# Optimization experiments

Measured on AMD Instinct MI355X. Metric: run time of the kernel, lower is better.

## Reference

```python
import jax, jax.numpy as jnp
import numpy as np

B_SZ, NP, NTOK, D, H, DH, D2 = 8192, 10, 21, 128, 2, 64, 32
EPS = 1e-8
PATCH_POS = np.array([2 * k - 1 for k in range(1, NP + 1)])  # [1,3,...,19]
STAT_POS = np.array([0] + [2 * k for k in range(1, NP + 1)])  # [0,2,...,20]


def setup_inputs() -> dict:
    key = jax.random.key(0)
    ks = jax.random.split(key, 12)
    x = jax.random.normal(ks[0], (B_SZ, NTOK, D), jnp.float32)
    # rotary frequencies: unit-magnitude complex exp(i * pos * theta)
    inv_freq = 1.0 / (10000.0 ** (jnp.arange(D2, dtype=jnp.float32) / D2))
    ang = jnp.arange(NTOK, dtype=jnp.float32)[:, None] * inv_freq[None, :]  # [N, d2]
    fc_real, fc_imag = jnp.cos(ang), jnp.sin(ang)
    s = 1.0 / np.sqrt(D)
    g = 1.0 + 0.02 * jax.random.normal(ks[1], (D,), jnp.float32)
    Wqkv = s * jax.random.normal(ks[2], (D, 3 * D), jnp.float32)
    bqkv = jnp.zeros((3 * D,), jnp.float32)
    Wout = s * jax.random.normal(ks[3], (D, D), jnp.float32)
    bout = jnp.zeros((D,), jnp.float32)
    Wg = s * jax.random.normal(ks[4], (D, D), jnp.float32)
    bg = jnp.zeros((D,), jnp.float32)
    Wr = s * jax.random.normal(ks[5], (D, D), jnp.float32)
    br = jnp.zeros((D,), jnp.float32)
    # learned bias B: decoupled init 0.0, coupled patch<->stat pairs 2.0
    Bb = np.zeros((NTOK, NTOK), np.float32)
    Bb[PATCH_POS, STAT_POS[1:]] = 2.0
    Bb[STAT_POS[1:], PATCH_POS] = 2.0
    return dict(x=x, fc_real=fc_real, fc_imag=fc_imag, g=g, Wqkv=Wqkv, bqkv=bqkv,
                Wout=Wout, bout=bout, Wg=Wg, bg=bg, Wr=Wr, br=br, Bbias=jnp.asarray(Bb))


def _zcrmsnorm(x, g):
    x0 = x - x.mean(-1, keepdims=True)
    return x0 / jnp.sqrt(jnp.mean(x0 * x0, -1, keepdims=True) + EPS) * g


def _rope(t, fr, fi):
    # t: [B,H,N,DH] viewed as complex pairs [B,H,N,d2,2]; fr/fi: [N,d2]
    tr = t.reshape(*t.shape[:-1], D2, 2)
    a, b = tr[..., 0], tr[..., 1]
    out = jnp.stack([a * fr - b * fi, a * fi + b * fr], axis=-1)
    return out.reshape(t.shape)


def reference(x, fc_real, fc_imag, g, Wqkv, bqkv, Wout, bout, Wg, bg, Wr, br, Bbias):
    B, N, Dm = x.shape
    h = _zcrmsnorm(x, g)
    qkv = (h @ Wqkv + bqkv).reshape(B, N, 3, H, DH)
    q = qkv[:, :, 0].transpose(0, 2, 1, 3)  # [B,H,N,DH]
    k = qkv[:, :, 1].transpose(0, 2, 1, 3)
    v = qkv[:, :, 2].transpose(0, 2, 1, 3)
    fr, fi = fc_real[:N], fc_imag[:N]
    q, k = _rope(q, fr, fi), _rope(k, fr, fi)
    scale = 1.0 / np.sqrt(DH)
    scores = jnp.einsum('bhnd,bhmd->bhnm', q, k) * scale + Bbias[None, None]
    a_full = jax.nn.softmax(scores, axis=-1)
    y_full = jnp.einsum('bhnm,bhmd->bhnd', a_full, v)
    y_full = y_full.transpose(0, 2, 1, 3).reshape(B, N, Dm) @ Wout + bout
    # patch -> stat attention
    q_p, k_s, v_s = q[:, :, PATCH_POS], k[:, :, STAT_POS], v[:, :, STAT_POS]
    sc2 = jnp.einsum('bhnd,bhmd->bhnm', q_p, k_s) * scale
    a2 = jax.nn.softmax(sc2, axis=-1)
    y2 = jnp.einsum('bhnm,bhmd->bhnd', a2, v_s).transpose(0, 2, 1, 3).reshape(B, NP, Dm)
    y2 = y2 @ Wr + br
    h_patch = h[:, PATCH_POS]  # [B,NP,D]
    norms = jnp.linalg.norm(h_patch, axis=-1, keepdims=True)
    uncertainty = 1.0 - jax.nn.sigmoid(norms - norms.mean())
    gate = jax.nn.sigmoid(h_patch @ Wg + bg) * uncertainty
    y = y_full.at[:, PATCH_POS, :].add(gate * y2)
    return x + y
```

## Files before the change

kernel.cpp:

```cpp
#include <hip/hip_runtime.h>
#include <math.h>

#define NB   8192
#define NTOK 21
#define NP   10

typedef _Float16 f16_t;
typedef _Float16 f16x8 __attribute__((ext_vector_type(8)));
typedef _Float16 f16x4 __attribute__((ext_vector_type(4)));
typedef float    f32x4 __attribute__((ext_vector_type(4)));

#define ROW128(r,c) ((r)*128 + ((c) ^ (((r)&7)<<3)))
#define VTIDX(d,m)  ((d)*32  + ((m) ^ (((d)&3)<<3)))
#define ATIDX(r,m)  ((r)*32  + ((m) ^ (((r)&3)<<3)))
#define TOK0(mt)    ((mt) ? 8 : 0)

#define MFMA(a,b,c) __builtin_amdgcn_mfma_f32_16x16x32_f16((a),(b),(c),0,0,0)

__global__ __launch_bounds__(256) void k_prep(
    const float* __restrict__ Wqkv, const float* __restrict__ Wout,
    const float* __restrict__ Wg,   const float* __restrict__ Wr,
    const float* __restrict__ x,    const float* __restrict__ g,
    f16_t* __restrict__ wq, f16_t* __restrict__ wo,
    f16_t* __restrict__ wgb, f16_t* __restrict__ wrb,
    float* __restrict__ part)
{
    __shared__ float sd[4];
    if (blockIdx.x < 384) {
        int i = blockIdx.x * 256 + threadIdx.x;
        if (i < 49152) {
            int k = i / 384, n = i - k * 384;
            wq[((k >> 3) * 384 + n) * 8 + (k & 7)] = (f16_t)Wqkv[i];
        } else {
            int j = i - 49152;
            int sel = j >> 14;
            int t = j & 16383;
            int k = t >> 7, n = t & 127;
            const float* src = sel == 0 ? Wout : (sel == 1 ? Wg : Wr);
            f16_t* dst = sel == 0 ? wo : (sel == 1 ? wgb : wrb);
            dst[((k >> 3) * 128 + n) * 8 + (k & 7)] = (f16_t)src[t];
        }
    } else {
        const int nb = blockIdx.x - 384;
        const int wave = threadIdx.x >> 6, lane = threadIdx.x & 63;
        const float g0v = g[lane], g1v = g[lane + 64];
        float acc = 0.f;
        #pragma unroll
        for (int rr = 0; rr < 8; rr++) {
            int row = nb * 32 + wave * 8 + rr;
            int b = row / NP, p = row - b * NP;
            const float* xr = x + (size_t)b * 2688 + (2 * p + 1) * 128;
            float a0 = xr[lane], a1 = xr[lane + 64];
            float s = a0 + a1, sq = a0 * a0 + a1 * a1;
            #pragma unroll
            for (int off = 32; off; off >>= 1) { s += __shfl_xor(s, off); sq += __shfl_xor(sq, off); }
            float mean = s * (1.0f / 128);
            float rstd = rsqrtf(sq * (1.0f / 128) - mean * mean + 1e-8f);
            float h0 = (a0 - mean) * rstd * g0v;
            float h1 = (a1 - mean) * rstd * g1v;
            float n2 = h0 * h0 + h1 * h1;
            #pragma unroll
            for (int off = 32; off; off >>= 1) n2 += __shfl_xor(n2, off);
            if (lane == 0) acc += sqrtf(n2);
        }
        if (lane == 0) sd[wave] = acc;
        __syncthreads();
        if (threadIdx.x == 0)
            atomicAdd(&part[(nb & 63) * 16], sd[0] + sd[1] + sd[2] + sd[3]);
    }
}

__global__ __launch_bounds__(256, 5) void k_main(
    const float* __restrict__ x,   const float* __restrict__ fcr,
    const float* __restrict__ fci, const float* __restrict__ g,
    const float* __restrict__ bqkv, const float* __restrict__ bout,
    const float* __restrict__ bg,   const float* __restrict__ br,
    const float* __restrict__ Bb,   const float* __restrict__ part,
    const f16_t* __restrict__ wq,  const f16_t* __restrict__ wo,
    const f16_t* __restrict__ wgb, const f16_t* __restrict__ wrb,
    float* __restrict__ out)
{
    __shared__ __align__(16) f16_t hsb[24 * 128];
    __shared__ __align__(16) f16_t reg1[24 * 128];
    __shared__ __align__(16) f16_t reg2[24 * 128];
    __shared__ __align__(16) f16_t reg3[128 * 32];
    __shared__ __align__(16) char  pool[5376];
    __shared__ float normv[11];

    float* fcs  = (float*)pool;
    float* fis  = (float*)pool + 672;

    const int tid = threadIdx.x;
    const int w = tid >> 6, l = tid & 63, l15 = l & 15, gq = l >> 4;
    const int b = blockIdx.x;
    const float* xb = x + (size_t)b * 2688;

    {
        const float4* c4 = (const float4*)fcr; float4* dc = (float4*)fcs;
        const float4* i4 = (const float4*)fci; float4* di = (float4*)fis;
        if (tid < 168) { dc[tid] = c4[tid]; di[tid] = i4[tid]; }
        f16x8 zz;
        #pragma unroll
        for (int j = 0; j < 8; j++) zz[j] = (f16_t)0.f;
        {
            f16x8* z = (f16x8*)reg3;
            z[tid] = zz; z[tid + 256] = zz;
        }
        if (tid < 48) {
            int r = 21 + (tid >> 4), c0 = (tid & 15) * 8;
            *(f16x8*)&hsb[ROW128(r, c0)] = zz;
        }
        if (tid < 64) {
            float s = part[tid * 16];
            #pragma unroll
            for (int off = 32; off; off >>= 1) s += __shfl_xor(s, off);
            if (tid == 0) normv[10] = s * (1.f / 81920.f);
        }
        const int gid = tid >> 4, lane16 = tid & 15;
        const int c0 = lane16 * 8;
        float4 ga = *(const float4*)&g[c0];
        float4 gb4 = *(const float4*)&g[c0 + 4];
        for (int r = gid; r < 21; r += 16) {
            float4 a4 = *(const float4*)&xb[r * 128 + c0];
            float4 b4 = *(const float4*)&xb[r * 128 + c0 + 4];
            float s  = a4.x + a4.y + a4.z + a4.w + b4.x + b4.y + b4.z + b4.w;
            float sq = a4.x*a4.x + a4.y*a4.y + a4.z*a4.z + a4.w*a4.w
                     + b4.x*b4.x + b4.y*b4.y + b4.z*b4.z + b4.w*b4.w;
            #pragma unroll
            for (int off = 8; off; off >>= 1) { s += __shfl_xor(s, off); sq += __shfl_xor(sq, off); }
            float mean = s * (1.0f / 128);
            float rstd = rsqrtf(sq * (1.0f / 128) - mean * mean + 1e-8f);
            float h[8];
            h[0]=(a4.x-mean)*rstd*ga.x;  h[1]=(a4.y-mean)*rstd*ga.y;
            h[2]=(a4.z-mean)*rstd*ga.z;  h[3]=(a4.w-mean)*rstd*ga.w;
            h[4]=(b4.x-mean)*rstd*gb4.x; h[5]=(b4.y-mean)*rstd*gb4.y;
            h[6]=(b4.z-mean)*rstd*gb4.z; h[7]=(b4.w-mean)*rstd*gb4.w;
            f16x8 hv;
            #pragma unroll
            for (int j = 0; j < 8; j++) hv[j] = (f16_t)h[j];
            *(f16x8*)&hsb[ROW128(r, c0)] = hv;
            if (r & 1) {
                float n2 = 0.f;
                #pragma unroll
                for (int j = 0; j < 8; j++) n2 += h[j] * h[j];
                #pragma unroll
                for (int off = 8; off; off >>= 1) n2 += __shfl_xor(n2, off);
                if (lane16 == 0) normv[r >> 1] = sqrtf(n2);
            }
        }
    }
    __syncthreads();

    {
        f16x8 afr[2][4];
        #pragma unroll
        for (int mt = 0; mt < 2; mt++)
            #pragma unroll
            for (int ks = 0; ks < 4; ks++)
                afr[mt][ks] = *(const f16x8*)&hsb[ROW128(TOK0(mt) + l15, ks * 32 + gq * 8)];
        #pragma unroll 2
        for (int q6 = 0; q6 < 6; ++q6) {
            int nt = w * 6 + q6;
            int n = nt * 16 + l15;
            f16x8 bfr[4];
            #pragma unroll
            for (int ks = 0; ks < 4; ks++)
                bfr[ks] = *(const f16x8*)&wq[((ks * 4 + gq) * 384 + n) * 8];
            float bias = bqkv[n];
            #pragma unroll
            for (int mt = 0; mt < 2; mt++) {
                f32x4 acc = {0.f, 0.f, 0.f, 0.f};
                #pragma unroll
                for (int ks = 0; ks < 4; ks++) acc = MFMA(afr[mt][ks], bfr[ks], acc);
                int rbase = TOK0(mt) + gq * 4;
                if (n < 256) {
                    int d = n & 63, j = d >> 1;
                    bool ev = !(d & 1);
                    f16_t* dst = (n < 128) ? reg1 : reg2;
                    int cc = n & 127;
                    #pragma unroll
                    for (int i = 0; i < 4; i++) {
                        int r = rbase + i; int rr = r < 21 ? r : 0;
                        float v = acc[i] + bias;
                        float p = __shfl_xor(v, 1);
                        float fr = fcs[rr * 32 + j], fi = fis[rr * 32 + j];
                        float o = ev ? (v * fr - p * fi) : (p * fi + v * fr);
                        dst[ROW128(r, cc)] = (f16_t)o;
                    }
                } else {
                    int d = n - 256;
                    f16x4 pv;
                    #pragma unroll
                    for (int i = 0; i < 4; i++) pv[i] = (f16_t)(acc[i] + bias);
                    *(f16x4*)&reg3[VTIDX(d, rbase)] = pv;
                }
            }
        }
    }
    __syncthreads();

    {
        f16_t* attb  = (f16_t*)pool;
        f16_t* att2e = (f16_t*)pool + 1536;
        {
            const int hh = w >> 1, mt = w & 1;
            const int b1row = (16 + l15 < 21) ? 16 + l15 : 20;
            f32x4 acc0 = {0.f, 0.f, 0.f, 0.f}, acc1 = {0.f, 0.f, 0.f, 0.f};
            #pragma unroll
            for (int ks = 0; ks < 2; ks++) {
                f16x8 a  = *(const f16x8*)&reg1[ROW128(TOK0(mt) + l15, hh * 64 + ks * 32 + gq * 8)];
                f16x8 b0 = *(const f16x8*)&reg2[ROW128(l15,            hh * 64 + ks * 32 + gq * 8)];
                f16x8 b1 = *(const f16x8*)&reg2[ROW128(b1row,          hh * 64 + ks * 32 + gq * 8)];
                acc0 = MFMA(a, b0, acc0);
                acc1 = MFMA(a, b1, acc1);
            }
            const int m0 = l15, m1 = 16 + l15;
            const bool c1 = (m1 < 21);
            #pragma unroll
            for (int i = 0; i < 4; i++) {
                int r = TOK0(mt) + gq * 4 + i;
                int rr = r < 21 ? r : 0;
                float v0 = acc0[i] * 0.125f + Bb[rr * 21 + m0];
                float v1 = c1 ? acc1[i] * 0.125f + Bb[rr * 21 + m1] : -1e30f;
                float mx = fmaxf(v0, v1);
                #pragma unroll
                for (int off = 8; off; off >>= 1) mx = fmaxf(mx, __shfl_xor(mx, off));
                float e0 = __expf(v0 - mx);
                float e1 = c1 ? __expf(v1 - mx) : 0.f;
                float s = e0 + e1;
                #pragma unroll
                for (int off = 8; off; off >>= 1) s += __shfl_xor(s, off);
                float is = 1.f / s;
                bool rv = (r < 21);
                attb[hh * 768 + ATIDX(r, m0)] = (f16_t)(rv ? e0 * is : 0.f);
                attb[hh * 768 + ATIDX(r, m1)] = (f16_t)(rv ? e1 * is : 0.f);
            }
        }
        if ((w & 1) == 0) {
            const int hh = w >> 1;
            int ra = 2 * l15 + 1; if (ra > 20) ra = 20;
            int rb = 2 * l15;     if (rb > 20) rb = 20;
            f32x4 acc = {0.f, 0.f, 0.f, 0.f};
            #pragma unroll
            for (int ks = 0; ks < 2; ks++) {
                f16x8 a  = *(const f16x8*)&reg1[ROW128(ra, hh * 64 + ks * 32 + gq * 8)];
                f16x8 bb = *(const f16x8*)&reg2[ROW128(rb, hh * 64 + ks * 32 + gq * 8)];
                acc = MFMA(a, bb, acc);
            }
            const bool cv = (l15 < 11);
            #pragma unroll
            for (int i = 0; i < 4; i++) {
                int p = gq * 4 + i;
                float v = cv ? acc[i] * 0.125f : -1e30f;
                float mx = v;
                #pragma unroll
                for (int off = 8; off; off >>= 1) mx = fmaxf(mx, __shfl_xor(mx, off));
                float e = cv ? __expf(v - mx) : 0.f;
                float s = e;
                #pragma unroll
                for (int off = 8; off; off >>= 1) s += __shfl_xor(s, off);
                float is = 1.f / s;
                att2e[hh * 512 + ATIDX(p, 2 * l15)]     = (f16_t)((p < 10) ? e * is : 0.f);
                att2e[hh * 512 + ATIDX(p, 2 * l15 + 1)] = (f16_t)0.f;
            }
        }
    }
    __syncthreads();

    {
        f16_t* attb  = (f16_t*)pool;
        f16_t* att2e = (f16_t*)pool + 1536;
        f16_t* y2bb  = reg1;
        for (int t = w * 6; t < w * 6 + 6; ++t) {
            int hh, dloc, mt = 0, isY2;
            if (t < 16) { hh = t >> 3; mt = (t >> 2) & 1; dloc = hh * 64 + (t & 3) * 16 + l15; isY2 = 0; }
            else        { int u = t - 16; hh = u >> 2;    dloc = hh * 64 + (u & 3) * 16 + l15; isY2 = 1; }
            f16x8 a;
            if (!isY2) { int r = TOK0(mt) + l15; a = *(const f16x8*)&attb[hh * 768 + ATIDX(r, gq * 8)]; }
            else       {                         a = *(const f16x8*)&att2e[hh * 512 + ATIDX(l15, gq * 8)]; }
            f16x8 bb = *(const f16x8*)&reg3[VTIDX(dloc, gq * 8)];
            f32x4 acc = {0.f, 0.f, 0.f, 0.f};
            acc = MFMA(a, bb, acc);
            if (!isY2) {
                #pragma unroll
                for (int i = 0; i < 4; i++) reg2[ROW128(TOK0(mt) + gq * 4 + i, dloc)] = (f16_t)acc[i];
            } else {
                #pragma unroll
                for (int i = 0; i < 4; i++) {
                    int rr2 = gq * 4 + i;
                    if (rr2 < 10) y2bb[ROW128(rr2, dloc)] = (f16_t)acc[i];
                }
            }
        }
    }
    __syncthreads();

    {
        f16_t* y2bb = reg1;
        float mn = normv[10];
        float* gyb = (float*)reg3;
        #pragma unroll
        for (int q2 = 0; q2 < 2; q2++) {
            int nt = w * 2 + q2;
            int n = nt * 16 + l15;
            int yrow = l15 < 10 ? l15 : 0;
            int hr   = l15 < 10 ? 2 * l15 + 1 : 1;
            f32x4 accg = {0.f, 0.f, 0.f, 0.f}, accr = {0.f, 0.f, 0.f, 0.f};
            #pragma unroll
            for (int ks = 0; ks < 4; ks++) {
                f16x8 wgf = *(const f16x8*)&wgb[((ks * 4 + gq) * 128 + n) * 8];
                f16x8 wrf = *(const f16x8*)&wrb[((ks * 4 + gq) * 128 + n) * 8];
                f16x8 ha  = *(const f16x8*)&hsb[ROW128(hr, ks * 32 + gq * 8)];
                f16x8 ya  = *(const f16x8*)&y2bb[ROW128(yrow, ks * 32 + gq * 8)];
                accg = MFMA(ha, wgf, accg);
                accr = MFMA(ya, wrf, accr);
            }
            float bgc = bg[n], brc = br[n];
            #pragma unroll
            for (int i = 0; i < 4; i++) {
                int p = gq * 4 + i;
                if (p < 10) {
                    float gate = 1.f / (1.f + __expf(-(accg[i] + bgc)));
                    float u = 1.f - 1.f / (1.f + __expf(-(normv[p] - mn)));
                    gyb[p * 128 + n] = u * gate * (accr[i] + brc);
                }
            }
        }
    }
    __syncthreads();

    {
        float* gyb = (float*)reg3;
        float* ob = out + (size_t)b * 2688;
        for (int t = w * 4; t < w * 4 + 4; ++t) {
            int mt = t >> 3, nt = t & 7;
            int n = nt * 16 + l15;
            f32x4 acc = {0.f, 0.f, 0.f, 0.f};
            #pragma unroll
            for (int ks = 0; ks < 4; ks++) {
                f16x8 a  = *(const f16x8*)&reg2[ROW128(TOK0(mt) + l15, ks * 32 + gq * 8)];
                f16x8 wf = *(const f16x8*)&wo[((ks * 4 + gq) * 128 + n) * 8];
                acc = MFMA(a, wf, acc);
            }
            float bo = bout[n];
            #pragma unroll
            for (int i = 0; i < 4; i++) {
                int r = TOK0(mt) + gq * 4 + i;
                if (r < 21) {
                    float v = xb[r * 128 + n] + acc[i] + bo;
                    if (r & 1) v += gyb[((r - 1) >> 1) * 128 + n];
                    ob[r * 128 + n] = v;
                }
            }
        }
    }
}

extern "C" void kernel_launch(void* const* d_in, const int* in_sizes, int n_in,
                              void* d_out, int out_size, void* d_ws, size_t ws_size,
                              hipStream_t stream)
{
    (void)in_sizes; (void)n_in; (void)out_size; (void)ws_size;
    const float* x    = (const float*)d_in[0];
    const float* fcr  = (const float*)d_in[1];
    const float* fci  = (const float*)d_in[2];
    const float* g    = (const float*)d_in[3];
    const float* Wqkv = (const float*)d_in[4];
    const float* bqkv = (const float*)d_in[5];
    const float* Wout = (const float*)d_in[6];
    const float* bout = (const float*)d_in[7];
    const float* Wg   = (const float*)d_in[8];
    const float* bg   = (const float*)d_in[9];
    const float* Wr   = (const float*)d_in[10];
    const float* br   = (const float*)d_in[11];
    const float* Bb   = (const float*)d_in[12];
    float* out = (float*)d_out;

    char* wsb = (char*)d_ws;
    float* part = (float*)wsb;
    f16_t* wq  = (f16_t*)(wsb + 4096);
    f16_t* wo  = wq + 49152;
    f16_t* wgb = wo + 16384;
    f16_t* wrb = wgb + 16384;

    hipMemsetAsync(part, 0, 4096, stream);
    hipLaunchKernelGGL(k_prep, dim3(2944), dim3(256), 0, stream,
                       Wqkv, Wout, Wg, Wr, x, g, wq, wo, wgb, wrb, part);
    hipLaunchKernelGGL(k_main, dim3(NB),   dim3(256), 0, stream,
                       x, fcr, fci, g, bqkv, bout, bg, br, Bb, part, wq, wo, wgb, wrb, out);
}
```

Measured before the change: 389.9 us.

## Prefetch weights and inputs into registers ahead of each stage, pad token tiles to 32

Global loads of weight fragments (Wqkv, Wg/Wr, Wout), the bias matrix and residual x are hoisted into registers one stage earlier, so their latency overlaps the preceding compute and barriers. The QKV loop is software-pipelined with double-buffered B fragments and fully unrolled. Token tiles change from overlapping rows 0-15 and 8-23 to disjoint rows 0-15 and 16-31, which grows the shared buffers. Occupancy is lowered from 5 to 4 blocks per CU to fit the extra registers and LDS.

```diff
diff --git a/kernel.cpp b/kernel.cpp
--- a/kernel.cpp
+++ b/kernel.cpp
@@ -13,7 +13,6 @@
 #define ROW128(r,c) ((r)*128 + ((c) ^ (((r)&7)<<3)))
 #define VTIDX(d,m)  ((d)*32  + ((m) ^ (((d)&3)<<3)))
 #define ATIDX(r,m)  ((r)*32  + ((m) ^ (((r)&3)<<3)))
-#define TOK0(mt)    ((mt) ? 8 : 0)
 
 #define MFMA(a,b,c) __builtin_amdgcn_mfma_f32_16x16x32_f16((a),(b),(c),0,0,0)
 
@@ -70,7 +69,7 @@
     }
 }
 
-__global__ __launch_bounds__(256, 5) void k_main(
+__global__ __launch_bounds__(256, 4) void k_main(
     const float* __restrict__ x,   const float* __restrict__ fcr,
     const float* __restrict__ fci, const float* __restrict__ g,
     const float* __restrict__ bqkv, const float* __restrict__ bout,
@@ -80,11 +79,11 @@
     const f16_t* __restrict__ wgb, const f16_t* __restrict__ wrb,
     float* __restrict__ out)
 {
-    __shared__ __align__(16) f16_t hsb[24 * 128];
-    __shared__ __align__(16) f16_t reg1[24 * 128];
-    __shared__ __align__(16) f16_t reg2[24 * 128];
+    __shared__ __align__(16) f16_t hsb[32 * 128];
+    __shared__ __align__(16) f16_t reg1[32 * 128];
+    __shared__ __align__(16) f16_t reg2[32 * 128];
     __shared__ __align__(16) f16_t reg3[128 * 32];
-    __shared__ __align__(16) char  pool[5376];
+    __shared__ __align__(16) char  pool[6144];
     __shared__ float normv[11];
 
     float* fcs  = (float*)pool;
@@ -95,6 +94,25 @@
     const int b = blockIdx.x;
     const float* xb = x + (size_t)b * 2688;
 
+    f16x8 bfr[4];
+    {
+        int n0p = (w * 6) * 16 + l15;
+        #pragma unroll
+        for (int ks = 0; ks < 4; ks++)
+            bfr[ks] = *(const f16x8*)&wq[((ks * 4 + gq) * 384 + n0p) * 8];
+    }
+    float bbv[8];
+    {
+        int mt = w & 1;
+        int m0 = l15, m1 = (16 + l15 < 21) ? 16 + l15 : 20;
+        #pragma unroll
+        for (int i = 0; i < 4; i++) {
+            int rr = mt * 16 + gq * 4 + i; rr = rr < 21 ? rr : 20;
+            bbv[i]     = Bb[rr * 21 + m0];
+            bbv[4 + i] = Bb[rr * 21 + m1];
+        }
+    }
+
     {
         const float4* c4 = (const float4*)fcr; float4* dc = (float4*)fcs;
         const float4* i4 = (const float4*)fci; float4* di = (float4*)fis;
@@ -106,7 +124,7 @@
             f16x8* z = (f16x8*)reg3;
             z[tid] = zz; z[tid + 256] = zz;
         }
-        if (tid < 48) {
+        if (tid < 176) {
             int r = 21 + (tid >> 4), c0 = (tid & 15) * 8;
             *(f16x8*)&hsb[ROW128(r, c0)] = zz;
         }
@@ -157,22 +175,27 @@
         for (int mt = 0; mt < 2; mt++)
             #pragma unroll
             for (int ks = 0; ks < 4; ks++)
-                afr[mt][ks] = *(const f16x8*)&hsb[ROW128(TOK0(mt) + l15, ks * 32 + gq * 8)];
-        #pragma unroll 2
+                afr[mt][ks] = *(const f16x8*)&hsb[ROW128(mt * 16 + l15, ks * 32 + gq * 8)];
+        #pragma unroll
         for (int q6 = 0; q6 < 6; ++q6) {
             int nt = w * 6 + q6;
             int n = nt * 16 + l15;
-            f16x8 bfr[4];
-            #pragma unroll
-            for (int ks = 0; ks < 4; ks++)
-                bfr[ks] = *(const f16x8*)&wq[((ks * 4 + gq) * 384 + n) * 8];
+            f16x8 bnext[4];
+            if (q6 < 5) {
+                #pragma unroll
+                for (int ks = 0; ks < 4; ks++)
+                    bnext[ks] = *(const f16x8*)&wq[((ks * 4 + gq) * 384 + (n + 16)) * 8];
+            } else {
+                #pragma unroll
+                for (int ks = 0; ks < 4; ks++) bnext[ks] = bfr[ks];
+            }
             float bias = bqkv[n];
             #pragma unroll
             for (int mt = 0; mt < 2; mt++) {
                 f32x4 acc = {0.f, 0.f, 0.f, 0.f};
                 #pragma unroll
                 for (int ks = 0; ks < 4; ks++) acc = MFMA(afr[mt][ks], bfr[ks], acc);
-                int rbase = TOK0(mt) + gq * 4;
+                int rbase = mt * 16 + gq * 4;
                 if (n < 256) {
                     int d = n & 63, j = d >> 1;
                     bool ev = !(d & 1);
@@ -195,22 +218,24 @@
                     *(f16x4*)&reg3[VTIDX(d, rbase)] = pv;
                 }
             }
+            #pragma unroll
+            for (int ks = 0; ks < 4; ks++) bfr[ks] = bnext[ks];
         }
     }
     __syncthreads();
 
     {
         f16_t* attb  = (f16_t*)pool;
-        f16_t* att2e = (f16_t*)pool + 1536;
+        f16_t* att2e = (f16_t*)pool + 2048;
         {
             const int hh = w >> 1, mt = w & 1;
             const int b1row = (16 + l15 < 21) ? 16 + l15 : 20;
             f32x4 acc0 = {0.f, 0.f, 0.f, 0.f}, acc1 = {0.f, 0.f, 0.f, 0.f};
             #pragma unroll
             for (int ks = 0; ks < 2; ks++) {
-                f16x8 a  = *(const f16x8*)&reg1[ROW128(TOK0(mt) + l15, hh * 64 + ks * 32 + gq * 8)];
-                f16x8 b0 = *(const f16x8*)&reg2[ROW128(l15,            hh * 64 + ks * 32 + gq * 8)];
-                f16x8 b1 = *(const f16x8*)&reg2[ROW128(b1row,          hh * 64 + ks * 32 + gq * 8)];
+                f16x8 a  = *(const f16x8*)&reg1[ROW128(mt * 16 + l15, hh * 64 + ks * 32 + gq * 8)];
+                f16x8 b0 = *(const f16x8*)&reg2[ROW128(l15,           hh * 64 + ks * 32 + gq * 8)];
+                f16x8 b1 = *(const f16x8*)&reg2[ROW128(b1row,         hh * 64 + ks * 32 + gq * 8)];
                 acc0 = MFMA(a, b0, acc0);
                 acc1 = MFMA(a, b1, acc1);
             }
@@ -218,10 +243,9 @@
             const bool c1 = (m1 < 21);
             #pragma unroll
             for (int i = 0; i < 4; i++) {
-                int r = TOK0(mt) + gq * 4 + i;
-                int rr = r < 21 ? r : 0;
-                float v0 = acc0[i] * 0.125f + Bb[rr * 21 + m0];
-                float v1 = c1 ? acc1[i] * 0.125f + Bb[rr * 21 + m1] : -1e30f;
+                int r = mt * 16 + gq * 4 + i;
+                float v0 = acc0[i] * 0.125f + bbv[i];
+                float v1 = c1 ? acc1[i] * 0.125f + bbv[4 + i] : -1e30f;
                 float mx = fmaxf(v0, v1);
                 #pragma unroll
                 for (int off = 8; off; off >>= 1) mx = fmaxf(mx, __shfl_xor(mx, off));
@@ -232,8 +256,8 @@
                 for (int off = 8; off; off >>= 1) s += __shfl_xor(s, off);
                 float is = 1.f / s;
                 bool rv = (r < 21);
-                attb[hh * 768 + ATIDX(r, m0)] = (f16_t)(rv ? e0 * is : 0.f);
-                attb[hh * 768 + ATIDX(r, m1)] = (f16_t)(rv ? e1 * is : 0.f);
+                attb[hh * 1024 + ATIDX(r, m0)] = (f16_t)(rv ? e0 * is : 0.f);
+                attb[hh * 1024 + ATIDX(r, m1)] = (f16_t)(rv ? e1 * is : 0.f);
             }
         }
         if ((w & 1) == 0) {
@@ -267,23 +291,24 @@
     }
     __syncthreads();
 
+    f16x8 wgf_pre[2][4], wrf_pre[2][4];
     {
         f16_t* attb  = (f16_t*)pool;
-        f16_t* att2e = (f16_t*)pool + 1536;
+        f16_t* att2e = (f16_t*)pool + 2048;
         f16_t* y2bb  = reg1;
         for (int t = w * 6; t < w * 6 + 6; ++t) {
             int hh, dloc, mt = 0, isY2;
             if (t < 16) { hh = t >> 3; mt = (t >> 2) & 1; dloc = hh * 64 + (t & 3) * 16 + l15; isY2 = 0; }
             else        { int u = t - 16; hh = u >> 2;    dloc = hh * 64 + (u & 3) * 16 + l15; isY2 = 1; }
             f16x8 a;
-            if (!isY2) { int r = TOK0(mt) + l15; a = *(const f16x8*)&attb[hh * 768 + ATIDX(r, gq * 8)]; }
-            else       {                         a = *(const f16x8*)&att2e[hh * 512 + ATIDX(l15, gq * 8)]; }
+            if (!isY2) { int r = mt * 16 + l15; a = *(const f16x8*)&attb[hh * 1024 + ATIDX(r, gq * 8)]; }
+            else       {                        a = *(const f16x8*)&att2e[hh * 512 + ATIDX(l15, gq * 8)]; }
             f16x8 bb = *(const f16x8*)&reg3[VTIDX(dloc, gq * 8)];
             f32x4 acc = {0.f, 0.f, 0.f, 0.f};
             acc = MFMA(a, bb, acc);
             if (!isY2) {
                 #pragma unroll
-                for (int i = 0; i < 4; i++) reg2[ROW128(TOK0(mt) + gq * 4 + i, dloc)] = (f16_t)acc[i];
+                for (int i = 0; i < 4; i++) reg2[ROW128(mt * 16 + gq * 4 + i, dloc)] = (f16_t)acc[i];
             } else {
                 #pragma unroll
                 for (int i = 0; i < 4; i++) {
@@ -292,9 +317,20 @@
                 }
             }
         }
+        #pragma unroll
+        for (int q2 = 0; q2 < 2; q2++) {
+            int n = (w * 2 + q2) * 16 + l15;
+            #pragma unroll
+            for (int ks = 0; ks < 4; ks++) {
+                wgf_pre[q2][ks] = *(const f16x8*)&wgb[((ks * 4 + gq) * 128 + n) * 8];
+                wrf_pre[q2][ks] = *(const f16x8*)&wrb[((ks * 4 + gq) * 128 + n) * 8];
+            }
+        }
     }
     __syncthreads();
 
+    f16x8 wo_pre[4][4];
+    float xv[4][4];
     {
         f16_t* y2bb = reg1;
         float mn = normv[10];
@@ -308,12 +344,10 @@
             f32x4 accg = {0.f, 0.f, 0.f, 0.f}, accr = {0.f, 0.f, 0.f, 0.f};
             #pragma unroll
             for (int ks = 0; ks < 4; ks++) {
-                f16x8 wgf = *(const f16x8*)&wgb[((ks * 4 + gq) * 128 + n) * 8];
-                f16x8 wrf = *(const f16x8*)&wrb[((ks * 4 + gq) * 128 + n) * 8];
                 f16x8 ha  = *(const f16x8*)&hsb[ROW128(hr, ks * 32 + gq * 8)];
                 f16x8 ya  = *(const f16x8*)&y2bb[ROW128(yrow, ks * 32 + gq * 8)];
-                accg = MFMA(ha, wgf, accg);
-                accr = MFMA(ya, wrf, accr);
+                accg = MFMA(ha, wgf_pre[q2][ks], accg);
+                accr = MFMA(ya, wrf_pre[q2][ks], accr);
             }
             float bgc = bg[n], brc = br[n];
             #pragma unroll
@@ -326,28 +360,43 @@
                 }
             }
         }
+        #pragma unroll
+        for (int t2 = 0; t2 < 4; t2++) {
+            int t = w * 4 + t2;
+            int mt = t >> 3, nt = t & 7;
+            int n = nt * 16 + l15;
+            #pragma unroll
+            for (int ks = 0; ks < 4; ks++)
+                wo_pre[t2][ks] = *(const f16x8*)&wo[((ks * 4 + gq) * 128 + n) * 8];
+            #pragma unroll
+            for (int i = 0; i < 4; i++) {
+                int r = mt * 16 + gq * 4 + i;
+                xv[t2][i] = (r < 21) ? xb[r * 128 + n] : 0.f;
+            }
+        }
     }
     __syncthreads();
 
     {
         float* gyb = (float*)reg3;
         float* ob = out + (size_t)b * 2688;
-        for (int t = w * 4; t < w * 4 + 4; ++t) {
+        #pragma unroll
+        for (int t2 = 0; t2 < 4; t2++) {
+            int t = w * 4 + t2;
             int mt = t >> 3, nt = t & 7;
             int n = nt * 16 + l15;
             f32x4 acc = {0.f, 0.f, 0.f, 0.f};
             #pragma unroll
             for (int ks = 0; ks < 4; ks++) {
-                f16x8 a  = *(const f16x8*)&reg2[ROW128(TOK0(mt) + l15, ks * 32 + gq * 8)];
-                f16x8 wf = *(const f16x8*)&wo[((ks * 4 + gq) * 128 + n) * 8];
-                acc = MFMA(a, wf, acc);
+                f16x8 a = *(const f16x8*)&reg2[ROW128(mt * 16 + l15, ks * 32 + gq * 8)];
+                acc = MFMA(a, wo_pre[t2][ks], acc);
             }
             float bo = bout[n];
             #pragma unroll
             for (int i = 0; i < 4; i++) {
-                int r = TOK0(mt) + gq * 4 + i;
+                int r = mt * 16 + gq * 4 + i;
                 if (r < 21) {
-                    float v = xb[r * 128 + n] + acc[i] + bo;
+                    float v = xv[t2][i] + acc[i] + bo;
                     if (r & 1) v += gyb[((r - 1) >> 1) * 128 + n];
                     ob[r * 128 + n] = v;
                 }
```

Measured after the change: 336.7 us. -13.7%, faster.
